# Optimization experiments

Hardware: AMD Instinct MI355X
Metric: run time of the kernel (lower is better)

The kernel has to match this reference:

```python
import jax, jax.numpy as jnp
import numpy as np

D = 1024      # d_model
H = 16        # n_heads
HD = D // H   # head_dim = 64
B = 2
T = 2048


def setup_inputs() -> dict:
    key = jax.random.key(0)
    k0, k1, k2 = jax.random.split(key, 3)
    s = 1.0 / np.sqrt(D)
    return {
        "x": jax.random.normal(k0, (B, T, D), dtype=jnp.float32),
        "qkv_w": jax.random.normal(k1, (D, 3 * D), dtype=jnp.float32) * s,
        "qkv_b": jnp.zeros((3 * D,), dtype=jnp.float32),
        "out_w": jax.random.normal(k2, (D, D), dtype=jnp.float32) * s,
        "out_b": jnp.zeros((D,), dtype=jnp.float32),
    }


def _apply_rotary(x, rope):
    # Faithful to the torch apply_rotary: even/odd interleaved split of both
    # x and the [sin(freqs)|cos(freqs)] rope table.
    x1, x2 = x[..., ::2], x[..., 1::2]
    sin, cos = rope[..., ::2], rope[..., 1::2]
    return jnp.concatenate([x1 * cos - x2 * sin, x1 * sin + x2 * cos], axis=-1)


def reference(x, qkv_w, qkv_b, out_w, out_b):
    Bx, Tx, Dm = x.shape
    # QKV projection -> [3, B, H, T, HD]
    qkv = (x @ qkv_w + qkv_b).reshape(Bx, Tx, 3, H, HD).transpose(2, 0, 3, 1, 4)
    q, k, v = qkv[0], qkv[1], qkv[2]

    # Rotary table: rope = concat(sin(freqs), cos(freqs)) along last dim -> [T, HD]
    inv_freq = 1.0 / (10000.0 ** (jnp.arange(0, HD, 2, dtype=jnp.float32) / HD))
    t = jnp.arange(Tx, dtype=jnp.float32)
    freqs = t[:, None] * inv_freq[None, :]          # [T, HD/2]
    rope = jnp.concatenate([jnp.sin(freqs), jnp.cos(freqs)], axis=-1)  # [T, HD]

    q = _apply_rotary(q, rope)
    k = _apply_rotary(k, rope)

    scale = HD ** -0.5
    scores = jnp.einsum('bhqd,bhkd->bhqk', q, k) * scale  # [B,H,T,T]
    causal_mask = jnp.triu(jnp.ones((Tx, Tx), dtype=bool), 1)
    scores = jnp.where(causal_mask, -jnp.inf, scores)
    attn = jax.nn.softmax(scores, axis=-1)
    # dropout is identity in eval mode
    out = jnp.einsum('bhqk,bhkd->bhqd', attn, v)           # [B,H,T,HD]
    out = out.transpose(0, 2, 1, 3).reshape(Bx, Tx, Dm)    # [B,T,D]
    return out @ out_w + out_b
```

## Files before the change

kernel.cpp:

```cpp
#include <hip/hip_runtime.h>

typedef unsigned short u16;
typedef __attribute__((ext_vector_type(8))) __bf16 bf16x8;
typedef __attribute__((ext_vector_type(4))) float f32x4;

#define NB 2
#define NT 2048
#define ND 1024
#define NH 16
#define HD 64

__device__ __forceinline__ float b2f(u16 u) {
  union { float f; unsigned int i; } v; v.i = ((unsigned int)u) << 16; return v.f;
}
__device__ __forceinline__ u16 f2b(float f) {
  union { float f; unsigned int i; } v; v.f = f;
  unsigned int r = (v.i + 0x7FFFu + ((v.i >> 16) & 1u)) >> 16;
  return (u16)r;
}
__device__ __forceinline__ unsigned int cvtpk(float lo, float hi) {
  unsigned int pk;
  asm("v_cvt_pk_bf16_f32 %0, %1, %2" : "=v"(pk) : "v"(lo), "v"(hi));
  return pk;
}

__device__ __forceinline__ void gload_lds16(const u16* g, u16* lds) {
  __builtin_amdgcn_global_load_lds(
      (const __attribute__((address_space(1))) unsigned int*)(g),
      (__attribute__((address_space(3))) unsigned int*)(lds),
      16, 0, 0);
}

__device__ __forceinline__ f32x4 mfma16(bf16x8 a, bf16x8 b, f32x4 c) {
  return __builtin_amdgcn_mfma_f32_16x16x32_bf16(a, b, c, 0, 0, 0);
}

template <int N>
__device__ __forceinline__ float ror16(float x) {
  return __int_as_float(__builtin_amdgcn_update_dpp(
      __float_as_int(x), __float_as_int(x), 0x120 | N, 0xF, 0xF, true));
}
__device__ __forceinline__ float rsum16(float x) {
  x += ror16<8>(x);
  x += ror16<4>(x);
  x += ror16<2>(x);
  x += ror16<1>(x);
  return x;
}

__device__ __forceinline__ float fast_sin(float a) {
  float r = a * 0.15915494309189535f;
  r -= floorf(r);
  return __builtin_amdgcn_sinf(r);
}
__device__ __forceinline__ float fast_cos(float a) {
  float r = a * 0.15915494309189535f;
  r -= floorf(r);
  return __builtin_amdgcn_cosf(r);
}

__global__ __launch_bounds__(256) void prep_inputs(
    const float* __restrict__ x, const float* __restrict__ qkv_w,
    const float* __restrict__ out_w, u16* __restrict__ xb,
    u16* __restrict__ wqkvT, u16* __restrict__ woutT) {
  __shared__ u16 tile[32][33];
  const int blk = blockIdx.x;
  const int tid = threadIdx.x;
  if (blk < 2048) {
    int i = (blk * 256 + tid) * 8;
#pragma unroll
    for (int j = 0; j < 8; ++j) xb[i + j] = f2b(x[i + j]);
    return;
  }
  const float* in; u16* out; int N; int idx;
  if (blk < 5120) { idx = blk - 2048; in = qkv_w; out = wqkvT; N = 3072; }
  else            { idx = blk - 5120; in = out_w; out = woutT; N = 1024; }
  const int nbx = N / 32;
  const int n0 = (idx % nbx) * 32, k0 = (idx / nbx) * 32;
  const int tx = tid & 31, ty = tid >> 5;
  for (int i2 = ty; i2 < 32; i2 += 8)
    tile[i2][tx] = f2b(in[(size_t)(k0 + i2) * N + n0 + tx]);
  __syncthreads();
  for (int i2 = ty; i2 < 32; i2 += 8)
    out[(size_t)(n0 + i2) * 1024 + k0 + tx] = tile[tx][i2];
}

__global__ __launch_bounds__(256, 2) void gemm128_2ph(const u16* __restrict__ A,
                                                      const u16* __restrict__ Bt,
                                                      const float* __restrict__ bias,
                                                      float* __restrict__ C,
                                                      int M, int N, int K) {
  __shared__ alignas(16) u16 lds[2][2][8192];
  const int tid = threadIdx.x;
  const int lane = tid & 63;
  const int wave = tid >> 6;
  const int l15 = lane & 15, quad = lane >> 4;
  const int wm = (wave >> 1) * 64, wn = (wave & 1) * 64;

  const int lin = blockIdx.y * gridDim.x + blockIdx.x;
  const int xcd = lin & 7, loc = lin >> 3;
  const int row0 = (xcd * 4 + (loc >> 3)) * 128;
  const int col0 = (loc & 7) * 128;

  const int sr = tid >> 3;
  const size_t soff = (size_t)sr * K + (size_t)((tid & 7) ^ (sr & 7)) * 8;
  const u16* Ab = A + (size_t)row0 * K;
  const u16* Bb = Bt + (size_t)col0 * K;

  const int swz0 = (quad ^ (l15 & 7)) * 8;
  const int swz1 = ((4 + quad) ^ (l15 & 7)) * 8;
  const int arow = (wm + l15) * 64;
  const int brow = (wn + l15) * 64;

  f32x4 acc[4][4] = {};
  const int NTIL = K >> 6;

#define STAGE8(dst, bptr, koff)                                              \
  _Pragma("unroll") for (int p = 0; p < 4; ++p)                              \
      gload_lds16((bptr) + (koff) + soff + (size_t)p * 32 * K,               \
                  &(dst)[(p * 256 + tid) * 8]);

  STAGE8(lds[0][0], Ab, 0);
  STAGE8(lds[0][1], Bb, 0);
  asm volatile("s_waitcnt vmcnt(0)");
  __builtin_amdgcn_s_barrier();
  asm volatile("" ::: "memory");

  for (int t = 0; t < NTIL; ++t) {
    const int cur = t & 1;
    if (t + 1 < NTIL) {
      STAGE8(lds[cur ^ 1][0], Ab, (size_t)(t + 1) * 64);
      STAGE8(lds[cur ^ 1][1], Bb, (size_t)(t + 1) * 64);
    }
    bf16x8 af[4][2], bfr[4][2];
#pragma unroll
    for (int i = 0; i < 4; ++i) {
      af[i][0]  = *(const bf16x8*)&lds[cur][0][arow + i * 1024 + swz0];
      af[i][1]  = *(const bf16x8*)&lds[cur][0][arow + i * 1024 + swz1];
      bfr[i][0] = *(const bf16x8*)&lds[cur][1][brow + i * 1024 + swz0];
      bfr[i][1] = *(const bf16x8*)&lds[cur][1][brow + i * 1024 + swz1];
    }
    asm volatile("s_waitcnt lgkmcnt(0)");
    __builtin_amdgcn_sched_barrier(0);
#pragma unroll
    for (int i = 0; i < 4; ++i)
#pragma unroll
      for (int j = 0; j < 4; ++j) {
        acc[i][j] = mfma16(af[i][0], bfr[j][0], acc[i][j]);
        acc[i][j] = mfma16(af[i][1], bfr[j][1], acc[i][j]);
      }
    asm volatile("s_waitcnt vmcnt(0)");
    __builtin_amdgcn_s_barrier();
    asm volatile("" ::: "memory");
  }
#undef STAGE8

#pragma unroll
  for (int j = 0; j < 4; ++j) {
    const int c = col0 + wn + j * 16 + l15;
    const float bv = bias[c];
#pragma unroll
    for (int i = 0; i < 4; ++i) {
      const int rr0 = row0 + wm + i * 16 + quad * 4;
      f32x4 v = acc[i][j];
#pragma unroll
      for (int rr = 0; rr < 4; ++rr)
        C[(size_t)(rr0 + rr) * N + c] = v[rr] + bv;
    }
  }
}

__device__ __forceinline__ void stage2(const u16* g0, const u16* g1, u16* l,
                                       int tid) {
  gload_lds16(g0, &l[tid * 8]);
  gload_lds16(g1, &l[(512 + tid) * 8]);
}

__device__ __forceinline__ u16* tsw(u16* base, int row, int col) {
  int byte = row * 512 + ((col * 2) ^ ((row & 15) << 4));
  return (u16*)((char*)base + byte);
}

#define AH(b, h) (&lds[((b) * 2 + (h)) * 8192])
#define BH(b, h) (&lds[32768 + ((b) * 2 + (h)) * 8192])

#define LOAD_AFX(dst, base)                                                 \
  _Pragma("unroll") for (int mm = 0; mm < 4; ++mm) {                        \
    dst[mm][0] = *(const bf16x8*)&(base)[arow + mm * 2048 + swz0];          \
    dst[mm][1] = *(const bf16x8*)&(base)[arow + mm * 2048 + swz1];          \
  }
#define LOAD_BF(base)                                                       \
  _Pragma("unroll") for (int nn = 0; nn < 2; ++nn) {                        \
    bfr[nn][0] = *(const bf16x8*)&(base)[brow + nn * 4096 + swz0];          \
    bfr[nn][1] = *(const bf16x8*)&(base)[brow + nn * 4096 + swz1];          \
  }
#define MFMA_QX(afv, MA, NQ)                                                \
  _Pragma("unroll") for (int mm = 0; mm < 4; ++mm)                          \
  _Pragma("unroll") for (int nn = 0; nn < 2; ++nn) {                        \
    acc[(MA) * 4 + mm][(NQ) * 2 + nn] =                                     \
        mfma16(afv[mm][0], bfr[nn][0], acc[(MA) * 4 + mm][(NQ) * 2 + nn]);  \
    acc[(MA) * 4 + mm][(NQ) * 2 + nn] =                                     \
        mfma16(afv[mm][1], bfr[nn][1], acc[(MA) * 4 + mm][(NQ) * 2 + nn]);  \
  }
#define PH_SYNC                                                             \
  __builtin_amdgcn_s_barrier();                                             \
  asm volatile("s_waitcnt lgkmcnt(0)");                                     \
  __builtin_amdgcn_sched_barrier(0);                                        \
  __builtin_amdgcn_s_setprio(1);
#define PH_END                                                              \
  __builtin_amdgcn_s_setprio(0);                                            \
  __builtin_amdgcn_s_barrier();                                             \
  asm volatile("" ::: "memory");

__global__ __launch_bounds__(512, 2) void gemm256_qkv(const u16* __restrict__ A,
                                                      const u16* __restrict__ Bt,
                                                      const float* __restrict__ bias,
                                                      u16* __restrict__ qsw,
                                                      u16* __restrict__ ksw,
                                                      u16* __restrict__ vsw,
                                                      int K) {
  __shared__ alignas(16) u16 lds[65536];
  const int tid = threadIdx.x;
  const int lane = tid & 63;
  const int wave = tid >> 6;
  const int l15 = lane & 15, quad = lane >> 4;
  const int wm = wave >> 2, wn = wave & 3;

  const int lin = blockIdx.y * gridDim.x + blockIdx.x;
  const int xcd = lin & 7, loc = lin >> 3;
  const int row0 = ((xcd & 3) * 4 + loc / 6) * 256;
  const int col0 = ((xcd >> 2) * 6 + loc % 6) * 256;
  const int NTIL = K >> 6;

  const int sr = tid >> 3;
  const size_t soff = (size_t)sr * K + (size_t)((tid & 7) ^ (sr & 7)) * 8;
  const size_t hK = (size_t)64 * K;
  const u16* A0p = A + (size_t)row0 * K + soff;
  const u16* A1p = A0p + 2 * hK;
  const u16* B0p = Bt + (size_t)col0 * K + soff;
  const u16* B1p = B0p + 2 * hK;

  const int swz0 = (quad ^ (l15 & 7)) * 8;
  const int swz1 = ((4 + quad) ^ (l15 & 7)) * 8;
  const int arow = (wm * 16 + l15) * 64;
  const int brow = (wn * 16 + l15) * 64;

  f32x4 acc[8][4] = {};

  stage2(B0p, B0p + hK, BH(0, 0), tid);
  stage2(A1p, A1p + hK, AH(0, 1), tid);
  stage2(A0p, A0p + hK, AH(0, 0), tid);
  stage2(B1p, B1p + hK, BH(0, 1), tid);
  {
    int tp = (NTIL > 1) ? 1 : 0;
    stage2(B0p + tp * 64, B0p + tp * 64 + hK, BH(1, 0), tid);
    stage2(A1p + tp * 64, A1p + tp * 64 + hK, AH(1, 1), tid);
  }
  asm volatile("s_waitcnt vmcnt(4)");
  __builtin_amdgcn_s_barrier();
  asm volatile("" ::: "memory");

  bf16x8 afA[4][2], afB[4][2], bfr[2][2];
#pragma unroll 2
  for (int t = 0; t < NTIL; ++t) {
    const int cur = t & 1, nxt = cur ^ 1;
    const int o1 = ((t + 1 < NTIL) ? t + 1 : NTIL - 1) * 64;
    const int o2 = ((t + 2 < NTIL) ? t + 2 : NTIL - 1) * 64;
    u16* Ac0 = AH(cur, 0);
    u16* Ac1 = AH(cur, 1);
    u16* Bc0 = BH(cur, 0);
    u16* Bc1 = BH(cur, 1);

    LOAD_AFX(afA, Ac0);
    LOAD_BF(Bc0);
    stage2(A0p + o1, A0p + o1 + hK, AH(nxt, 0), tid);
    PH_SYNC; MFMA_QX(afA, 0, 0); PH_END;

    LOAD_AFX(afB, Ac1);
    stage2(B1p + o1, B1p + o1 + hK, BH(nxt, 1), tid);
    PH_SYNC; MFMA_QX(afB, 1, 0); PH_END;

    LOAD_BF(Bc1);
    stage2(B0p + o2, B0p + o2 + hK, Bc0, tid);
    PH_SYNC; MFMA_QX(afB, 1, 1); PH_END;

    stage2(A1p + o2, A1p + o2 + hK, Ac1, tid);
    __builtin_amdgcn_s_barrier();
    __builtin_amdgcn_sched_barrier(0);
    __builtin_amdgcn_s_setprio(1);
    MFMA_QX(afA, 0, 1);
    __builtin_amdgcn_s_setprio(0);
    asm volatile("s_waitcnt vmcnt(4)");
    __builtin_amdgcn_s_barrier();
    asm volatile("" ::: "memory");
  }
  asm volatile("s_waitcnt vmcnt(0)");
  __syncthreads();

#pragma unroll
  for (int ni = 0; ni < 4; ++ni) {
    const int col_in = (ni >> 1) * 128 + (ni & 1) * 64 + wn * 16 + l15;
    const float bv = bias[col0 + col_in];
#pragma unroll
    for (int mi = 0; mi < 8; ++mi) {
      const int r_in0 = (mi >> 2) * 128 + (mi & 3) * 32 + wm * 16 + quad * 4;
      f32x4 v = acc[mi][ni];
#pragma unroll
      for (int rr = 0; rr < 4; ++rr)
        *tsw(lds, r_in0 + rr, col_in) = f2b(v[rr] + bv);
    }
  }
  __syncthreads();

  const int tt = col0 >> 10;
  const int h0 = (col0 & 1023) >> 6;
  const int bb = row0 >> 11;
  const int tb0 = row0 & 2047;

  if (tt < 2) {
    u16* dst = (tt == 0) ? qsw : ksw;
    const float scale = (tt == 0) ? 0.125f : 1.0f;
    const float LOG1E4 = 9.210340371976184f;
    const int hh = tid >> 7;
    const int chunk = (tid >> 4) & 7;
    const int tl = tid & 15;
    const int ks = chunk >> 2, qd = chunk & 3;
    const int bh = bb * 16 + h0 + hh;
    float inv1a[8], inv2a[8];
    int cc[8], c1a[8], c2a[8];
#pragma unroll
    for (int e = 0; e < 8; ++e) {
      int c = ks * 32 + qd * 8 + e;
      int j = c & 31;
      cc[e] = c; c1a[e] = 2 * j; c2a[e] = 2 * j + 1;
      inv1a[e] = __expf(-((float)(c1a[e] & 31)) * (1.0f / 32.0f) * LOG1E4);
      inv2a[e] = __expf(-((float)(c2a[e] & 31)) * (1.0f / 32.0f) * LOG1E4);
    }
    for (int tb = 0; tb < 8; ++tb) {
      const int tbt = tb0 + tb * 32;
#pragma unroll
      for (int rbloc = 0; rbloc < 2; ++rbloc) {
        const int rrow = tb * 32 + rbloc * 16 + tl;
        const float tf = (float)(tbt + rbloc * 16 + tl);
        union { u16 s[8]; unsigned int u[4]; bf16x8 v; } o;
        float ovv[8];
#pragma unroll
        for (int e = 0; e < 8; ++e) {
          float a1 = tf * inv1a[e], a2 = tf * inv2a[e];
          float sA = (c1a[e] < 32) ? fast_sin(a1) : fast_cos(a1);
          float cA = (c2a[e] < 32) ? fast_sin(a2) : fast_cos(a2);
          float x1 = b2f(*tsw(lds, rrow, hh * 64 + c1a[e]));
          float x2 = b2f(*tsw(lds, rrow, hh * 64 + c2a[e]));
          float ov = (cc[e] < 32) ? (x1 * cA - x2 * sA) : (x1 * sA + x2 * cA);
          ovv[e] = ov * scale;
        }
#pragma unroll
        for (int p2 = 0; p2 < 4; ++p2)
          o.u[p2] = cvtpk(ovv[2 * p2], ovv[2 * p2 + 1]);
        size_t addr =
            ((((size_t)bh * 128 + (tbt >> 4) + rbloc) * 2 + ks) * 64 +
             qd * 16 + tl) * 8;
        *(bf16x8*)&dst[addr] = o.v;
      }
    }
  } else {
    const int u = tid >> 8;
    const int utid = tid & 255;
    const int ni = utid >> 6, lane2 = utid & 63;
    const int qd = lane2 >> 4, l15b = lane2 & 15;
    for (int it = 0; it < 16; ++it) {
      const int unit = it * 2 + u;
      const int hh = unit >> 3, tb = unit & 7;
      const int bh = bb * 16 + h0 + hh;
      const int tbt = tb0 + tb * 32;
      union { u16 s[8]; bf16x8 v; } o;
#pragma unroll
      for (int e = 0; e < 8; ++e) {
        int p = qd * 8 + e;
        int krow = (p >> 1) + ((p & 1) << 4);
        o.s[e] = *tsw(lds, tb * 32 + krow, hh * 64 + ni * 16 + l15b);
      }
      *(bf16x8*)&vsw[(((size_t)bh * 64 + (tbt >> 5)) * 4 + ni) * 512 +
                     lane2 * 8] = o.v;
    }
  }
}

__global__ __launch_bounds__(128, 2) void flash_kernel(const u16* __restrict__ qsw,
                                                       const u16* __restrict__ ksw,
                                                       const u16* __restrict__ vsw,
                                                       u16* __restrict__ attn) {
  __shared__ alignas(16) u16 Ps[2 * 5120];
  float* const Of = (float*)&Ps[5120];
  float* const Ll = (float*)&Ps[9216];

  const int tid = threadIdx.x;
  const int w = tid >> 6;
  const int lane = tid & 63;
  const int l15 = lane & 15, quad = lane >> 4;
  const int linear = (int)blockIdx.x;
  const int bh = linear & 31;
  const int qt = 63 - (linear >> 5);
  const int r0 = qt * 32;
  u16* Psw = &Ps[w * 5120];

  bf16x8 aq[2][2];
#pragma unroll
  for (int mi = 0; mi < 2; ++mi)
#pragma unroll
    for (int ks = 0; ks < 2; ++ks)
      aq[mi][ks] = *(const bf16x8*)&qsw[
          ((((size_t)bh * 128 + qt * 2 + mi) * 2 + ks) * 64 + lane) * 8];

  f32x4 oacc[2][4] = {};
  float lst[8] = {0.f, 0.f, 0.f, 0.f, 0.f, 0.f, 0.f, 0.f};

  const int ktmax = qt >> 2;
  for (int kt = w; kt <= ktmax; kt += 2) {
    bf16x8 kf[2][8];
#pragma unroll
    for (int ks = 0; ks < 2; ++ks)
#pragma unroll
      for (int ni = 0; ni < 8; ++ni)
        kf[ks][ni] = *(const bf16x8*)&ksw[
            ((((size_t)bh * 128 + kt * 8 + ni) * 2 + ks) * 64 + lane) * 8];

    f32x4 sacc[2][8] = {};
#pragma unroll
    for (int ks = 0; ks < 2; ++ks)
#pragma unroll
      for (int ni = 0; ni < 8; ++ni) {
        sacc[0][ni] = mfma16(aq[0][ks], kf[ks][ni], sacc[0][ni]);
        sacc[1][ni] = mfma16(aq[1][ks], kf[ks][ni], sacc[1][ni]);
      }

    bf16x8 vf[4][4];
#pragma unroll
    for (int ks = 0; ks < 4; ++ks)
#pragma unroll
      for (int ni = 0; ni < 4; ++ni)
        vf[ks][ni] = *(const bf16x8*)&vsw[
            (((size_t)bh * 64 + kt * 4 + ks) * 4 + ni) * 512 + lane * 8];

    const bool diag = (kt == ktmax);
    const int k0 = kt * 128;
#pragma unroll
    for (int mi = 0; mi < 2; ++mi)
#pragma unroll
      for (int r = 0; r < 4; ++r) {
        const int prow = mi * 16 + quad * 4 + r;
        float sv[8];
#pragma unroll
        for (int ni = 0; ni < 8; ++ni) sv[ni] = sacc[mi][ni][r];
        if (diag) {
#pragma unroll
          for (int ni = 0; ni < 8; ++ni)
            if (k0 + ni * 16 + l15 > r0 + prow) sv[ni] = -__builtin_inff();
        }
        float rs = 0.f;
#pragma unroll
        for (int ni = 0; ni < 8; ++ni) {
          float p = __expf(sv[ni]);
          sv[ni] = p;
          rs += p;
        }
        lst[mi * 4 + r] += rsum16(rs);
#pragma unroll
        for (int ni = 0; ni < 8; ni += 2) {
          unsigned int pk = cvtpk(sv[ni], sv[ni + 1]);
          *(unsigned int*)&Psw[(ni >> 1) * 1280 + prow * 40 + 2 * l15] = pk;
        }
      }

    asm volatile("" ::: "memory");

#pragma unroll
    for (int ks = 0; ks < 4; ++ks) {
      bf16x8 ap0 = *(const bf16x8*)&Psw[ks * 1280 + l15 * 40 + quad * 8];
      bf16x8 ap1 = *(const bf16x8*)&Psw[ks * 1280 + (16 + l15) * 40 + quad * 8];
#pragma unroll
      for (int ni = 0; ni < 4; ++ni) {
        oacc[0][ni] = mfma16(ap0, vf[ks][ni], oacc[0][ni]);
        oacc[1][ni] = mfma16(ap1, vf[ks][ni], oacc[1][ni]);
      }
    }
  }

  if (w == 1) {
#pragma unroll
    for (int mi = 0; mi < 2; ++mi)
#pragma unroll
      for (int r = 0; r < 4; ++r) {
        const int row = mi * 16 + quad * 4 + r;
        if (l15 == 0) Ll[row] = lst[mi * 4 + r];
#pragma unroll
        for (int ni = 0; ni < 4; ++ni)
          Of[row * 64 + ni * 16 + l15] = oacc[mi][ni][r];
      }
  }
  __syncthreads();
  if (w == 0) {
    const int b = bh >> 4, h = bh & 15;
#pragma unroll
    for (int mi = 0; mi < 2; ++mi)
#pragma unroll
      for (int r = 0; r < 4; ++r) {
        const int row = mi * 16 + quad * 4 + r;
        const float rl = 1.0f / (lst[mi * 4 + r] + Ll[row]);
        const int trow = r0 + row;
#pragma unroll
        for (int ni = 0; ni < 4; ++ni) {
          float o = oacc[mi][ni][r] + Of[row * 64 + ni * 16 + l15];
          attn[((size_t)b * NT + trow) * ND + h * HD + ni * 16 + l15] = f2b(o * rl);
        }
      }
  }
}

extern "C" void kernel_launch(void* const* d_in, const int* in_sizes, int n_in,
                              void* d_out, int out_size, void* d_ws, size_t ws_size,
                              hipStream_t stream) {
  const float* x = (const float*)d_in[0];
  const float* qkv_w = (const float*)d_in[1];
  const float* qkv_b = (const float*)d_in[2];
  const float* out_w = (const float*)d_in[3];
  const float* out_b = (const float*)d_in[4];
  float* out = (float*)d_out;

  u16* ws = (u16*)d_ws;
  u16* xb    = ws;
  u16* wqkvT = xb + (size_t)4096 * 1024;
  u16* woutT = wqkvT + 3072 * 1024;
  u16* qsw   = woutT + 1024 * 1024;
  u16* ksw   = qsw + (size_t)32 * 2048 * 64;
  u16* vsw   = ksw + (size_t)32 * 2048 * 64;
  u16* attn  = vsw + (size_t)32 * 2048 * 64;

  prep_inputs<<<dim3(6144), 256, 0, stream>>>(x, qkv_w, out_w, xb, wqkvT, woutT);

  gemm256_qkv<<<dim3(12, 16), 512, 0, stream>>>(
      xb, wqkvT, qkv_b, qsw, ksw, vsw, ND);

  flash_kernel<<<dim3(2048), 128, 0, stream>>>(qsw, ksw, vsw, attn);

  gemm128_2ph<<<dim3(ND / 128, NB * NT / 128), 256, 0, stream>>>(
      attn, woutT, out_b, out, NB * NT, ND, ND);
}
```

Before: 179.8 us.

## Precompute rotary sin/cos table and shrink output GEMM tile to 64 rows

Adds a rotary sin/cos table to the prep kernel. The QKV GEMM epilogue now reads precomputed sin/cos values and vectorized LDS rows, instead of evaluating exp, sin and cos per element. Separately, the output projection GEMM uses 64x128 tiles with three blocks per CU, giving 512 blocks instead of 256 for better occupancy and wave balance. The cost is extra global reads for the table, plus lower reuse per tile in the output GEMM.

```diff
diff --git a/kernel.cpp b/kernel.cpp
--- a/kernel.cpp
+++ b/kernel.cpp
@@ -62,7 +62,8 @@
 __global__ __launch_bounds__(256) void prep_inputs(
     const float* __restrict__ x, const float* __restrict__ qkv_w,
     const float* __restrict__ out_w, u16* __restrict__ xb,
-    u16* __restrict__ wqkvT, u16* __restrict__ woutT) {
+    u16* __restrict__ wqkvT, u16* __restrict__ woutT,
+    float* __restrict__ rtab) {
   __shared__ u16 tile[32][33];
   const int blk = blockIdx.x;
   const int tid = threadIdx.x;
@@ -70,6 +71,19 @@
     int i = (blk * 256 + tid) * 8;
 #pragma unroll
     for (int j = 0; j < 8; ++j) xb[i + j] = f2b(x[i + j]);
+    return;
+  }
+  if (blk >= 6144) {
+    const float LOG1E4 = 9.210340371976184f;
+    int base = (blk - 6144) * 4096 + tid * 16;
+#pragma unroll
+    for (int j = 0; j < 16; ++j) {
+      int idx = base + j;
+      int t = idx >> 6, c = idx & 63;
+      float inv = __expf(-((float)(c & 31)) * (1.0f / 32.0f) * LOG1E4);
+      float a = (float)t * inv;
+      rtab[idx] = (c < 32) ? fast_sin(a) : fast_cos(a);
+    }
     return;
   }
   const float* in; u16* out; int N; int idx;
@@ -85,21 +99,22 @@
     out[(size_t)(n0 + i2) * 1024 + k0 + tx] = tile[tx][i2];
 }
 
-__global__ __launch_bounds__(256, 2) void gemm128_2ph(const u16* __restrict__ A,
-                                                      const u16* __restrict__ Bt,
-                                                      const float* __restrict__ bias,
-                                                      float* __restrict__ C,
-                                                      int M, int N, int K) {
-  __shared__ alignas(16) u16 lds[2][2][8192];
+__global__ __launch_bounds__(256, 3) void gemm64_2ph(const u16* __restrict__ A,
+                                                     const u16* __restrict__ Bt,
+                                                     const float* __restrict__ bias,
+                                                     float* __restrict__ C,
+                                                     int M, int N, int K) {
+  __shared__ alignas(16) u16 As[2][4096];
+  __shared__ alignas(16) u16 Bs[2][8192];
   const int tid = threadIdx.x;
   const int lane = tid & 63;
   const int wave = tid >> 6;
   const int l15 = lane & 15, quad = lane >> 4;
-  const int wm = (wave >> 1) * 64, wn = (wave & 1) * 64;
+  const int wm = (wave >> 1) * 32, wn = (wave & 1) * 64;
 
   const int lin = blockIdx.y * gridDim.x + blockIdx.x;
   const int xcd = lin & 7, loc = lin >> 3;
-  const int row0 = (xcd * 4 + (loc >> 3)) * 128;
+  const int row0 = (xcd * 8 + (loc >> 3)) * 64;
   const int col0 = (loc & 7) * 128;
 
   const int sr = tid >> 3;
@@ -112,16 +127,20 @@
   const int arow = (wm + l15) * 64;
   const int brow = (wn + l15) * 64;
 
-  f32x4 acc[4][4] = {};
+  f32x4 acc[2][4] = {};
   const int NTIL = K >> 6;
 
-#define STAGE8(dst, bptr, koff)                                              \
+#define STAGEA(buf, koff)                                                    \
+  _Pragma("unroll") for (int p = 0; p < 2; ++p)                              \
+      gload_lds16(Ab + (koff) + soff + (size_t)p * 32 * K,                   \
+                  &As[buf][(p * 256 + tid) * 8]);
+#define STAGEB(buf, koff)                                                    \
   _Pragma("unroll") for (int p = 0; p < 4; ++p)                              \
-      gload_lds16((bptr) + (koff) + soff + (size_t)p * 32 * K,               \
-                  &(dst)[(p * 256 + tid) * 8]);
-
-  STAGE8(lds[0][0], Ab, 0);
-  STAGE8(lds[0][1], Bb, 0);
+      gload_lds16(Bb + (koff) + soff + (size_t)p * 32 * K,                   \
+                  &Bs[buf][(p * 256 + tid) * 8]);
+
+  STAGEA(0, 0);
+  STAGEB(0, 0);
   asm volatile("s_waitcnt vmcnt(0)");
   __builtin_amdgcn_s_barrier();
   asm volatile("" ::: "memory");
@@ -129,21 +148,24 @@
   for (int t = 0; t < NTIL; ++t) {
     const int cur = t & 1;
     if (t + 1 < NTIL) {
-      STAGE8(lds[cur ^ 1][0], Ab, (size_t)(t + 1) * 64);
-      STAGE8(lds[cur ^ 1][1], Bb, (size_t)(t + 1) * 64);
-    }
-    bf16x8 af[4][2], bfr[4][2];
-#pragma unroll
-    for (int i = 0; i < 4; ++i) {
-      af[i][0]  = *(const bf16x8*)&lds[cur][0][arow + i * 1024 + swz0];
-      af[i][1]  = *(const bf16x8*)&lds[cur][0][arow + i * 1024 + swz1];
-      bfr[i][0] = *(const bf16x8*)&lds[cur][1][brow + i * 1024 + swz0];
-      bfr[i][1] = *(const bf16x8*)&lds[cur][1][brow + i * 1024 + swz1];
+      STAGEA(cur ^ 1, (size_t)(t + 1) * 64);
+      STAGEB(cur ^ 1, (size_t)(t + 1) * 64);
+    }
+    bf16x8 af[2][2], bfr[4][2];
+#pragma unroll
+    for (int i = 0; i < 2; ++i) {
+      af[i][0] = *(const bf16x8*)&As[cur][arow + i * 1024 + swz0];
+      af[i][1] = *(const bf16x8*)&As[cur][arow + i * 1024 + swz1];
+    }
+#pragma unroll
+    for (int j = 0; j < 4; ++j) {
+      bfr[j][0] = *(const bf16x8*)&Bs[cur][brow + j * 1024 + swz0];
+      bfr[j][1] = *(const bf16x8*)&Bs[cur][brow + j * 1024 + swz1];
     }
     asm volatile("s_waitcnt lgkmcnt(0)");
     __builtin_amdgcn_sched_barrier(0);
 #pragma unroll
-    for (int i = 0; i < 4; ++i)
+    for (int i = 0; i < 2; ++i)
 #pragma unroll
       for (int j = 0; j < 4; ++j) {
         acc[i][j] = mfma16(af[i][0], bfr[j][0], acc[i][j]);
@@ -153,14 +175,15 @@
     __builtin_amdgcn_s_barrier();
     asm volatile("" ::: "memory");
   }
-#undef STAGE8
+#undef STAGEA
+#undef STAGEB
 
 #pragma unroll
   for (int j = 0; j < 4; ++j) {
     const int c = col0 + wn + j * 16 + l15;
     const float bv = bias[c];
 #pragma unroll
-    for (int i = 0; i < 4; ++i) {
+    for (int i = 0; i < 2; ++i) {
       const int rr0 = row0 + wm + i * 16 + quad * 4;
       f32x4 v = acc[i][j];
 #pragma unroll
@@ -218,6 +241,7 @@
                                                       u16* __restrict__ qsw,
                                                       u16* __restrict__ ksw,
                                                       u16* __restrict__ vsw,
+                                                      const float* __restrict__ rope_tab,
                                                       int K) {
   __shared__ alignas(16) u16 lds[65536];
   const int tid = threadIdx.x;
@@ -320,38 +344,40 @@
   if (tt < 2) {
     u16* dst = (tt == 0) ? qsw : ksw;
     const float scale = (tt == 0) ? 0.125f : 1.0f;
-    const float LOG1E4 = 9.210340371976184f;
     const int hh = tid >> 7;
     const int chunk = (tid >> 4) & 7;
     const int tl = tid & 15;
     const int ks = chunk >> 2, qd = chunk & 3;
     const int bh = bb * 16 + h0 + hh;
-    float inv1a[8], inv2a[8];
-    int cc[8], c1a[8], c2a[8];
-#pragma unroll
-    for (int e = 0; e < 8; ++e) {
-      int c = ks * 32 + qd * 8 + e;
-      int j = c & 31;
-      cc[e] = c; c1a[e] = 2 * j; c2a[e] = 2 * j + 1;
-      inv1a[e] = __expf(-((float)(c1a[e] & 31)) * (1.0f / 32.0f) * LOG1E4);
-      inv2a[e] = __expf(-((float)(c2a[e] & 31)) * (1.0f / 32.0f) * LOG1E4);
-    }
+    const bool low = (ks == 0);
+    const int cbase = qd * 16;
+    const int xbyte0 = (hh * 64 + cbase) * 2;
+    const int sw = tl << 4;
     for (int tb = 0; tb < 8; ++tb) {
       const int tbt = tb0 + tb * 32;
 #pragma unroll
       for (int rbloc = 0; rbloc < 2; ++rbloc) {
         const int rrow = tb * 32 + rbloc * 16 + tl;
-        const float tf = (float)(tbt + rbloc * 16 + tl);
+        const int tg = tbt + rbloc * 16 + tl;
+        const char* rowp = (const char*)lds + rrow * 512;
+        bf16x8 q0 = *(const bf16x8*)(rowp + (xbyte0 ^ sw));
+        bf16x8 q1 = *(const bf16x8*)(rowp + ((xbyte0 + 16) ^ sw));
+        const float* tp = &rope_tab[tg * 64 + cbase];
+        float sc[16];
+        *(f32x4*)&sc[0]  = *(const f32x4*)(tp);
+        *(f32x4*)&sc[4]  = *(const f32x4*)(tp + 4);
+        *(f32x4*)&sc[8]  = *(const f32x4*)(tp + 8);
+        *(f32x4*)&sc[12] = *(const f32x4*)(tp + 12);
+        u16 xs[16];
+        *(bf16x8*)&xs[0] = q0;
+        *(bf16x8*)&xs[8] = q1;
         union { u16 s[8]; unsigned int u[4]; bf16x8 v; } o;
         float ovv[8];
 #pragma unroll
         for (int e = 0; e < 8; ++e) {
-          float a1 = tf * inv1a[e], a2 = tf * inv2a[e];
-          float sA = (c1a[e] < 32) ? fast_sin(a1) : fast_cos(a1);
-          float cA = (c2a[e] < 32) ? fast_sin(a2) : fast_cos(a2);
-          float x1 = b2f(*tsw(lds, rrow, hh * 64 + c1a[e]));
-          float x2 = b2f(*tsw(lds, rrow, hh * 64 + c2a[e]));
-          float ov = (cc[e] < 32) ? (x1 * cA - x2 * sA) : (x1 * sA + x2 * cA);
+          float x1 = b2f(xs[2 * e]), x2 = b2f(xs[2 * e + 1]);
+          float sA = sc[2 * e], cA = sc[2 * e + 1];
+          float ov = low ? (x1 * cA - x2 * sA) : (x1 * sA + x2 * cA);
           ovv[e] = ov * scale;
         }
 #pragma unroll
@@ -535,14 +561,16 @@
   u16* ksw   = qsw + (size_t)32 * 2048 * 64;
   u16* vsw   = ksw + (size_t)32 * 2048 * 64;
   u16* attn  = vsw + (size_t)32 * 2048 * 64;
-
-  prep_inputs<<<dim3(6144), 256, 0, stream>>>(x, qkv_w, out_w, xb, wqkvT, woutT);
+  float* rtab = (float*)(attn + (size_t)4096 * 1024);
+
+  prep_inputs<<<dim3(6176), 256, 0, stream>>>(
+      x, qkv_w, out_w, xb, wqkvT, woutT, rtab);
 
   gemm256_qkv<<<dim3(12, 16), 512, 0, stream>>>(
-      xb, wqkvT, qkv_b, qsw, ksw, vsw, ND);
+      xb, wqkvT, qkv_b, qsw, ksw, vsw, rtab, ND);
 
   flash_kernel<<<dim3(2048), 128, 0, stream>>>(qsw, ksw, vsw, attn);
 
-  gemm128_2ph<<<dim3(ND / 128, NB * NT / 128), 256, 0, stream>>>(
+  gemm64_2ph<<<dim3(ND / 128, NB * NT / 64), 256, 0, stream>>>(
       attn, woutT, out_b, out, NB * NT, ND, ND);
 }
```

New measurement: 179.0 us (median of 2 runs). Within noise of the previous version (-0.4%).
